# Performance work log

Hardware: AMD Instinct MI355X
Metric: run time of the kernel (lower is better)

## Reference

```python
import jax, jax.numpy as jnp
import numpy as np

N_NODES = 200000
N_GRAPHS = 4000


def _sage_conv(x, src, dst, W_l, b_l, W_r, num_nodes):
    # PyG SAGEConv (aggr='mean'): out = lin_l(mean_{j in N(i)} x_j) + lin_r(x_i)
    msg_sum = jax.ops.segment_sum(x[src], dst, num_segments=num_nodes)      # [N, d]
    deg = jax.ops.segment_sum(jnp.ones_like(src, dtype=x.dtype), dst,
                              num_segments=num_nodes)                       # [N]
    mean_nbr = msg_sum / jnp.maximum(deg, 1.0)[:, None]
    return mean_nbr @ W_l.T + b_l + x @ W_r.T


def setup_inputs() -> dict:
    key = jax.random.key(0)
    ks = jax.random.split(key, 10)
    in_ch, hid, out = 32, 64, 2
    E = 3200000
    x = jax.random.normal(ks[0], (N_NODES, in_ch), dtype=jnp.float32)
    edge_index = jax.random.randint(ks[1], (2, E), 0, N_NODES, dtype=jnp.int64)
    batch = jnp.sort(jax.random.randint(ks[2], (N_NODES,), 0, N_GRAPHS, dtype=jnp.int64))

    def glorot(k, shape):
        lim = 1.0 / np.sqrt(shape[1])
        return jax.random.uniform(k, shape, jnp.float32, -lim, lim)

    return {
        "x": x,
        "edge_index": edge_index,
        "batch": batch,
        "W1_l": glorot(ks[3], (hid, in_ch)),
        "b1": jnp.zeros((hid,), jnp.float32),
        "W1_r": glorot(ks[4], (hid, in_ch)),
        "W2_l": glorot(ks[5], (hid, hid)),
        "b2": jnp.zeros((hid,), jnp.float32),
        "W2_r": glorot(ks[6], (hid, hid)),
        "W_lin": glorot(ks[7], (out, hid)),
        "b_lin": jnp.zeros((out,), jnp.float32),
    }


def reference(x, edge_index, batch, W1_l, b1, W1_r, W2_l, b2, W2_r, W_lin, b_lin):
    src, dst = edge_index[0], edge_index[1]
    h = jax.nn.relu(_sage_conv(x, src, dst, W1_l, b1, W1_r, N_NODES))
    h = jax.nn.relu(_sage_conv(h, src, dst, W2_l, b2, W2_r, N_NODES))
    # global_mean_pool over graph ids
    pool_sum = jax.ops.segment_sum(h, batch, num_segments=N_GRAPHS)          # [G, 64]
    cnt = jax.ops.segment_sum(jnp.ones_like(batch, dtype=h.dtype), batch,
                              num_segments=N_GRAPHS)                          # [G]
    pooled = pool_sum / jnp.maximum(cnt, 1.0)[:, None]
    return pooled @ W_lin.T + b_lin
```

## Files before the change

### kernel.cpp

```cpp
#include <hip/hip_runtime.h>
#include <hip/hip_bf16.h>


#define WS_ALIGN 64
#define EPB 4096
#define BSHIFT 8
#define BNODES 256
#define BCAP 6144
#define MAXNB 1024

typedef short bf16x8 __attribute__((ext_vector_type(8)));
typedef float f32x4 __attribute__((ext_vector_type(4)));

__device__ inline unsigned short f2bf(float f) {
    unsigned u = __float_as_uint(f);
    return (unsigned short)((u + 0x7fffu + ((u >> 16) & 1u)) >> 16);
}

__device__ inline void acc8(const uint4 u, float* a) {
    a[0] += __uint_as_float(u.x << 16);
    a[1] += __uint_as_float(u.x & 0xffff0000u);
    a[2] += __uint_as_float(u.y << 16);
    a[3] += __uint_as_float(u.y & 0xffff0000u);
    a[4] += __uint_as_float(u.z << 16);
    a[5] += __uint_as_float(u.z & 0xffff0000u);
    a[6] += __uint_as_float(u.w << 16);
    a[7] += __uint_as_float(u.w & 0xffff0000u);
}


__global__ void prep_kernel(const float* __restrict__ x, unsigned short* __restrict__ xb,
                            const float* __restrict__ W1_l, const float* __restrict__ W1_r,
                            const float* __restrict__ W2_l, const float* __restrict__ W2_r,
                            unsigned short* __restrict__ whi1, unsigned short* __restrict__ whi2,
                            int* __restrict__ bucketCursor, float* __restrict__ pool,
                            int N, int NB, int G, int total4) {
    const int gid = blockIdx.x * blockDim.x + threadIdx.x;
    if (gid < total4) {
        const float4 v = reinterpret_cast<const float4*>(x)[gid];
        ushort4 o;
        o.x = f2bf(v.x); o.y = f2bf(v.y); o.z = f2bf(v.z); o.w = f2bf(v.w);
        reinterpret_cast<ushort4*>(xb)[gid] = o;
    }
    if (gid < NB) bucketCursor[gid] = gid * BCAP;
    if (gid < G * 64) pool[gid] = 0.0f;
    if (gid < 64 * 64) {
        const int o = gid >> 6, k = gid & 63;
        const float v = (k < 32) ? W1_l[o * 32 + k] : W1_r[o * 32 + (k - 32)];
        whi1[gid] = f2bf(v);
    }
    if (gid < 64 * 128) {
        const int o = gid >> 7, k = gid & 127;
        const float v = (k < 64) ? W2_l[o * 64 + k] : W2_r[o * 64 + (k - 64)];
        whi2[gid] = f2bf(v);
    }
}


__global__ __launch_bounds__(256) void bucket_scatter_kernel(const int* __restrict__ src,
                                                             const int* __restrict__ dst,
                                                             int* __restrict__ bucketCursor,
                                                             unsigned* __restrict__ bucketData,
                                                             int E, int NB) {
    __shared__ int hist[MAXNB];
    __shared__ int cur[MAXNB];
    const int t = threadIdx.x;
    for (int i = t; i < MAXNB; i += 256) hist[i] = 0;
    __syncthreads();
    const int eBase = blockIdx.x * EPB + t;
    int s[16], b[16], dl[16];
#pragma unroll
    for (int j = 0; j < 16; ++j) {
        int e = eBase + j * 256;
        if (e < E) {
            int d = dst[e];
            s[j]  = src[e];
            b[j]  = d >> BSHIFT;
            dl[j] = d & (BNODES - 1);
            atomicAdd(&hist[b[j]], 1);
        } else {
            b[j] = -1;
        }
    }
    __syncthreads();
    for (int bb = t; bb < NB; bb += 256)
        if (hist[bb] > 0) cur[bb] = atomicAdd(&bucketCursor[bb], hist[bb]);
    __syncthreads();
#pragma unroll
    for (int j = 0; j < 16; ++j) {
        if (b[j] >= 0) {
            int pos = atomicAdd(&cur[b[j]], 1);
            if (pos < (b[j] + 1) * BCAP)
                bucketData[pos] = ((unsigned)s[j] << BSHIFT) | (unsigned)dl[j];
        }
    }
}

__global__ __launch_bounds__(256) void csr_build_kernel(const unsigned* __restrict__ bucketData,
                                                        const int* __restrict__ bucketCursor,
                                                        int* __restrict__ offs,
                                                        int* __restrict__ offe,
                                                        int* __restrict__ csr_src,
                                                        int N) {
    __shared__ int cnt[BNODES];
    __shared__ int sscan[BNODES];
    __shared__ int cur[BNODES];
    const int t   = threadIdx.x;
    const int bkt = blockIdx.x;
    const int nodeBase = bkt << BSHIFT;
    const int regionBase = bkt * BCAP;
    const int count = min(bucketCursor[bkt] - regionBase, BCAP);
    cnt[t] = 0;
    __syncthreads();
    for (int k = regionBase + t; k < regionBase + count; k += 256)
        atomicAdd(&cnt[bucketData[k] & (BNODES - 1)], 1);
    __syncthreads();
    int v0 = cnt[t];
    sscan[t] = v0;
    __syncthreads();
    for (int off = 1; off < 256; off <<= 1) {
        int v = (t >= off) ? sscan[t - off] : 0;
        __syncthreads();
        sscan[t] += v;
        __syncthreads();
    }
    const int excl = sscan[t] - v0;
    cur[t] = excl;
    const int node = nodeBase + t;
    if (node < N) {
        offs[node] = regionBase + excl;
        offe[node] = regionBase + excl + v0;
    }
    __syncthreads();
    for (int k = regionBase + t; k < regionBase + count; k += 256) {
        const unsigned v = bucketData[k];
        const int d = (int)(v & (BNODES - 1));
        const int pos = regionBase + atomicAdd(&cur[d], 1);
        csr_src[pos] = (int)(v >> BSHIFT);
    }
}


template <int DIN, bool POOL>
__launch_bounds__(256)
__global__ void fused_agg_mfma_kernel(const unsigned short* __restrict__ featb,
                                      const unsigned short* __restrict__ whi,
                                      const float* __restrict__ bias,
                                      const int* __restrict__ csr_src,
                                      const int* __restrict__ offs,
                                      const int* __restrict__ offe,
                                      unsigned short* __restrict__ houtb,
                                      const int* __restrict__ batch,
                                      float* __restrict__ pool_sum,
                                      int N, int nSteps) {
    constexpr int K     = 2 * DIN;
    constexpr int STR   = K + 8;
    constexpr int D8    = DIN / 8;
    constexpr int NPW   = 64 / D8;
    constexpr int NPASS = 16 / NPW;
    __shared__ unsigned short A_s[64 * STR];
    __shared__ float poolLds[POOL ? 16 * 65 : 1];
    const int tid  = threadIdx.x;
    const int lane = tid & 63;
    const int wave = tid >> 6;
    const int nodeBase = blockIdx.x * 64;
    const int rowBase  = wave * 16;

    if (POOL) {
        for (int i = tid; i < 16 * 65; i += 256) poolLds[i] = 0.0f;
        __syncthreads();
    }

    for (int i = lane; i < 16 * D8; i += 64) {
        const int row = rowBase + i / D8, q = i % D8;
        const int n = min(nodeBase + row, N - 1);
        const uint4 u = *reinterpret_cast<const uint4*>(featb + (size_t)n * DIN + q * 8);
        *reinterpret_cast<uint4*>(&A_s[row * STR + DIN + q * 8]) = u;
    }

    {
        const int part = lane % D8;
        const uint4* base = reinterpret_cast<const uint4*>(featb);
#pragma unroll
        for (int pass = 0; pass < NPASS; ++pass) {
            const int row = rowBase + pass * NPW + lane / D8;
            const int n = nodeBase + row;
            unsigned short* dp = &A_s[row * STR + part * 8];
            if (n < N) {
                const int beg = offs[n];
                const int end = offe[n];
                float a[8] = {0.f, 0.f, 0.f, 0.f, 0.f, 0.f, 0.f, 0.f};
                int k = beg;
                for (; k + 8 <= end; k += 8) {
                    int s[8];
#pragma unroll
                    for (int j = 0; j < 8; ++j) s[j] = csr_src[k + j];
                    uint4 u[8];
#pragma unroll
                    for (int j = 0; j < 8; ++j) u[j] = base[(size_t)s[j] * D8 + part];
#pragma unroll
                    for (int j = 0; j < 8; ++j) acc8(u[j], a);
                }
                for (; k + 4 <= end; k += 4) {
                    const int s0 = csr_src[k + 0];
                    const int s1 = csr_src[k + 1];
                    const int s2 = csr_src[k + 2];
                    const int s3 = csr_src[k + 3];
                    const uint4 u0 = base[(size_t)s0 * D8 + part];
                    const uint4 u1 = base[(size_t)s1 * D8 + part];
                    const uint4 u2 = base[(size_t)s2 * D8 + part];
                    const uint4 u3 = base[(size_t)s3 * D8 + part];
                    acc8(u0, a); acc8(u1, a); acc8(u2, a); acc8(u3, a);
                }
                for (; k < end; ++k) {
                    const uint4 u = base[(size_t)csr_src[k] * D8 + part];
                    acc8(u, a);
                }
                const float inv = 1.0f / fmaxf((float)(end - beg), 1.0f);
                ushort4 lo4, hi4;
                lo4.x = f2bf(a[0] * inv); lo4.y = f2bf(a[1] * inv);
                lo4.z = f2bf(a[2] * inv); lo4.w = f2bf(a[3] * inv);
                hi4.x = f2bf(a[4] * inv); hi4.y = f2bf(a[5] * inv);
                hi4.z = f2bf(a[6] * inv); hi4.w = f2bf(a[7] * inv);
                *reinterpret_cast<ushort4*>(dp)     = lo4;
                *reinterpret_cast<ushort4*>(dp + 4) = hi4;
            } else {
                const ushort4 z = {0, 0, 0, 0};
                *reinterpret_cast<ushort4*>(dp)     = z;
                *reinterpret_cast<ushort4*>(dp + 4) = z;
            }
        }
    }

    asm volatile("s_waitcnt lgkmcnt(0)" ::: "memory");
    __builtin_amdgcn_sched_barrier(0);

    const int lr = lane & 15;
    const int q  = lane >> 4;
    f32x4 acc[4];
#pragma unroll
    for (int t = 0; t < 4; ++t) {
        const float b = bias[t * 16 + lr];
        acc[t] = (f32x4){b, b, b, b};
    }
    const unsigned short* Arow = &A_s[(rowBase + lr) * STR + q * 8];
    const unsigned short* Brow = whi + (size_t)lr * K + q * 8;
    for (int s = 0; s < nSteps; ++s) {
        const bf16x8 af = *reinterpret_cast<const bf16x8*>(Arow + s * 32);
#pragma unroll
        for (int t = 0; t < 4; ++t) {
            const bf16x8 bh = *reinterpret_cast<const bf16x8*>(
                Brow + (size_t)t * 16 * K + s * 32);
            acc[t] = __builtin_amdgcn_mfma_f32_16x16x32_bf16(af, bh, acc[t], 0, 0, 0);
        }
    }

    if (POOL) {
        const int g0 = batch[nodeBase];
        float ag[4] = {0.f, 0.f, 0.f, 0.f};
        int gcur = -1;
        auto flush_run = [&](int g) {
            const int r = g - g0;
            if (r < 16) {
#pragma unroll
                for (int t = 0; t < 4; ++t)
                    atomicAdd(&poolLds[r * 65 + t * 16 + lr], ag[t]);
            } else {
#pragma unroll
                for (int t = 0; t < 4; ++t)
                    atomicAdd(&pool_sum[(size_t)g * 64 + t * 16 + lr], ag[t]);
            }
        };
        for (int reg = 0; reg < 4; ++reg) {
            const int n = nodeBase + rowBase + q * 4 + reg;
            if (n >= N) break;
            const int g = batch[n];
            if (g != gcur) {
                if (gcur >= 0) flush_run(gcur);
                gcur = g;
                ag[0] = ag[1] = ag[2] = ag[3] = 0.f;
            }
#pragma unroll
            for (int t = 0; t < 4; ++t)
                ag[t] += fmaxf(acc[t][reg], 0.0f);
        }
        if (gcur >= 0) flush_run(gcur);
        __syncthreads();
        const int glast = batch[min(nodeBase + 63, N - 1)];
        const int S = min(glast - g0 + 1, 16);
        for (int i = tid; i < S * 64; i += 256) {
            const int r = i >> 6, c = i & 63;
            const float v = poolLds[r * 65 + c];
            float* dstp = &pool_sum[(size_t)(g0 + r) * 64 + c];
            if (r == 0 || r == S - 1) atomicAdd(dstp, v);
            else *dstp = v;
        }
    } else {
        for (int reg = 0; reg < 4; ++reg) {
            const int n = nodeBase + rowBase + q * 4 + reg;
            if (n >= N) break;
#pragma unroll
            for (int t = 0; t < 4; ++t)
                houtb[(size_t)n * 64 + t * 16 + lr] = f2bf(fmaxf(acc[t][reg], 0.0f));
        }
    }
}


__device__ inline int lower_bound_batch(const int* __restrict__ batch, int N, int key) {
    int lo = 0, hi = N;
    while (lo < hi) {
        const int mid = (lo + hi) >> 1;
        if (batch[mid] < key) lo = mid + 1; else hi = mid;
    }
    return lo;
}

__global__ void final_kernel(const float* __restrict__ pool_sum,
                             const int* __restrict__ batch,
                             const float* __restrict__ W_lin,
                             const float* __restrict__ b_lin,
                             float* __restrict__ out, int G, int N) {
    int t = blockIdx.x * blockDim.x + threadIdx.x;
    if (t >= G * 2) return;
    int g = t >> 1, o = t & 1;
    const int c0 = lower_bound_batch(batch, N, g);
    const int c1 = lower_bound_batch(batch, N, g + 1);
    float inv = 1.0f / fmaxf((float)(c1 - c0), 1.0f);
    float acc = b_lin[o];
#pragma unroll
    for (int c = 0; c < 64; ++c)
        acc = fmaf(pool_sum[(size_t)g * 64 + c] * inv, W_lin[o * 64 + c], acc);
    out[t] = acc;
}

extern "C" void kernel_launch(void* const* d_in, const int* in_sizes, int n_in,
                              void* d_out, int out_size, void* d_ws, size_t ws_size,
                              hipStream_t stream) {
    const float* x     = (const float*)d_in[0];
    const int*   ei    = (const int*)d_in[1];
    const int*   batch = (const int*)d_in[2];
    const float* W1_l  = (const float*)d_in[3];
    const float* b1    = (const float*)d_in[4];
    const float* W1_r  = (const float*)d_in[5];
    const float* W2_l  = (const float*)d_in[6];
    const float* b2    = (const float*)d_in[7];
    const float* W2_r  = (const float*)d_in[8];
    const float* W_lin = (const float*)d_in[9];
    const float* b_lin = (const float*)d_in[10];

    const int N = in_sizes[0] / 32;
    const int E = in_sizes[1] / 2;
    const int G = out_size / 2;
    const int* src = ei;
    const int* dst = ei + E;
    const int NB = (N + BNODES - 1) >> BSHIFT;

    char* p = (char*)d_ws;
    auto carve = [&](size_t bytes) -> void* {
        void* r = (void*)p;
        p += (bytes + (WS_ALIGN - 1)) / WS_ALIGN * WS_ALIGN;
        return r;
    };
    int*            bucketCursor = (int*)carve((size_t)MAXNB * 4);
    unsigned*       bucketData   = (unsigned*)carve((size_t)NB * BCAP * 4);
    int*            offs         = (int*)carve((size_t)N * 4);
    int*            offe         = (int*)carve((size_t)N * 4);
    int*            csr_src      = (int*)carve((size_t)NB * BCAP * 4);
    unsigned short* xb           = (unsigned short*)carve((size_t)N * 32 * 2);
    unsigned short* h1b          = (unsigned short*)carve((size_t)N * 64 * 2);
    unsigned short* whi1         = (unsigned short*)carve(64 * 64 * 2);
    unsigned short* whi2         = (unsigned short*)carve(64 * 128 * 2);
    float*          pool         = (float*)carve((size_t)G * 64 * 4);
    float*          out          = (float*)d_out;

    const int TB = 256;
    const int total4 = N * 32 / 4;
    prep_kernel<<<(total4 + TB - 1) / TB, TB, 0, stream>>>(
        x, xb, W1_l, W1_r, W2_l, W2_r, whi1, whi2, bucketCursor, pool,
        N, NB, G, total4);
    bucket_scatter_kernel<<<(E + EPB - 1) / EPB, TB, 0, stream>>>(src, dst, bucketCursor,
                                                                  bucketData, E, NB);
    csr_build_kernel<<<NB, TB, 0, stream>>>(bucketData, bucketCursor, offs, offe, csr_src, N);

    fused_agg_mfma_kernel<32, false><<<(N + 63) / 64, TB, 0, stream>>>(
        xb, whi1, b1, csr_src, offs, offe, h1b, nullptr, nullptr, N, 2);

    fused_agg_mfma_kernel<64, true><<<(N + 63) / 64, TB, 0, stream>>>(
        h1b, whi2, b2, csr_src, offs, offe, nullptr, batch, pool, N, 4);

    final_kernel<<<(G * 2 + TB - 1) / TB, TB, 0, stream>>>(pool, batch, W_lin, b_lin,
                                                           out, G, N);
}
```

Before: 337.0 us.

## Stage bucket scatter and CSR build in LDS for coalesced global writes

The bucket scatter kernel now sorts each block's edge records locally by bucket in shared memory, using a prefix scan over the histogram. It then writes them to global memory in bucket-contiguous order, replacing the earlier random per-edge stores. The CSR build kernel caches the bucket region in LDS, so global memory is read once instead of twice, and it permutes in LDS before writing csr_src out coalesced. This adds significant LDS use: about 48KB in each kernel, which may reduce occupancy. It also adds extra syncthreads and scan passes.

```diff
diff --git a/kernel.cpp b/kernel.cpp
--- a/kernel.cpp
+++ b/kernel.cpp
@@ -63,36 +63,68 @@
                                                              unsigned* __restrict__ bucketData,
                                                              int E, int NB) {
     __shared__ int hist[MAXNB];
-    __shared__ int cur[MAXNB];
+    __shared__ int lofs[MAXNB];
+    __shared__ int lcur[MAXNB];
+    __shared__ int gbase[MAXNB];
+    __shared__ int sscan[256];
+    __shared__ unsigned staged[EPB];
+    __shared__ int gaddr[EPB];
     const int t = threadIdx.x;
     for (int i = t; i < MAXNB; i += 256) hist[i] = 0;
     __syncthreads();
     const int eBase = blockIdx.x * EPB + t;
-    int s[16], b[16], dl[16];
+    int bkt[16]; unsigned rec[16];
 #pragma unroll
     for (int j = 0; j < 16; ++j) {
-        int e = eBase + j * 256;
+        const int e = eBase + j * 256;
         if (e < E) {
-            int d = dst[e];
-            s[j]  = src[e];
-            b[j]  = d >> BSHIFT;
-            dl[j] = d & (BNODES - 1);
-            atomicAdd(&hist[b[j]], 1);
+            const int d = dst[e];
+            bkt[j] = d >> BSHIFT;
+            rec[j] = ((unsigned)src[e] << BSHIFT) | (unsigned)(d & (BNODES - 1));
+            atomicAdd(&hist[bkt[j]], 1);
         } else {
-            b[j] = -1;
-        }
-    }
-    __syncthreads();
+            bkt[j] = -1;
+        }
+    }
+    __syncthreads();
+    const int b4 = t * 4;
+    const int h0 = hist[b4], h1 = hist[b4 + 1], h2 = hist[b4 + 2], h3 = hist[b4 + 3];
+    const int tsum = h0 + h1 + h2 + h3;
+    sscan[t] = tsum;
+    __syncthreads();
+    for (int off = 1; off < 256; off <<= 1) {
+        const int v = (t >= off) ? sscan[t - off] : 0;
+        __syncthreads();
+        sscan[t] += v;
+        __syncthreads();
+    }
+    const int excl = sscan[t] - tsum;
+    lofs[b4]     = excl;
+    lofs[b4 + 1] = excl + h0;
+    lofs[b4 + 2] = excl + h0 + h1;
+    lofs[b4 + 3] = excl + h0 + h1 + h2;
+    lcur[b4]     = lofs[b4];
+    lcur[b4 + 1] = lofs[b4 + 1];
+    lcur[b4 + 2] = lofs[b4 + 2];
+    lcur[b4 + 3] = lofs[b4 + 3];
     for (int bb = t; bb < NB; bb += 256)
-        if (hist[bb] > 0) cur[bb] = atomicAdd(&bucketCursor[bb], hist[bb]);
+        if (hist[bb] > 0) gbase[bb] = atomicAdd(&bucketCursor[bb], hist[bb]);
     __syncthreads();
 #pragma unroll
     for (int j = 0; j < 16; ++j) {
-        if (b[j] >= 0) {
-            int pos = atomicAdd(&cur[b[j]], 1);
-            if (pos < (b[j] + 1) * BCAP)
-                bucketData[pos] = ((unsigned)s[j] << BSHIFT) | (unsigned)dl[j];
-        }
+        if (bkt[j] >= 0) {
+            const int b = bkt[j];
+            const int lp = atomicAdd(&lcur[b], 1);
+            staged[lp] = rec[j];
+            const int gp = gbase[b] + (lp - lofs[b]);
+            gaddr[lp] = (gp < (b + 1) * BCAP) ? gp : -1;
+        }
+    }
+    __syncthreads();
+    const int cnt = min(EPB, E - blockIdx.x * EPB);
+    for (int i = t; i < cnt; i += 256) {
+        const int p = gaddr[i];
+        if (p >= 0) bucketData[p] = staged[i];
     }
 }
 
@@ -102,6 +134,8 @@
                                                         int* __restrict__ offe,
                                                         int* __restrict__ csr_src,
                                                         int N) {
+    __shared__ unsigned ldsIn[BCAP];
+    __shared__ unsigned ldsOut[BCAP];
     __shared__ int cnt[BNODES];
     __shared__ int sscan[BNODES];
     __shared__ int cur[BNODES];
@@ -112,14 +146,17 @@
     const int count = min(bucketCursor[bkt] - regionBase, BCAP);
     cnt[t] = 0;
     __syncthreads();
-    for (int k = regionBase + t; k < regionBase + count; k += 256)
-        atomicAdd(&cnt[bucketData[k] & (BNODES - 1)], 1);
-    __syncthreads();
-    int v0 = cnt[t];
+    for (int k = t; k < count; k += 256) {
+        const unsigned v = bucketData[regionBase + k];
+        ldsIn[k] = v;
+        atomicAdd(&cnt[v & (BNODES - 1)], 1);
+    }
+    __syncthreads();
+    const int v0 = cnt[t];
     sscan[t] = v0;
     __syncthreads();
     for (int off = 1; off < 256; off <<= 1) {
-        int v = (t >= off) ? sscan[t - off] : 0;
+        const int v = (t >= off) ? sscan[t - off] : 0;
         __syncthreads();
         sscan[t] += v;
         __syncthreads();
@@ -132,12 +169,14 @@
         offe[node] = regionBase + excl + v0;
     }
     __syncthreads();
-    for (int k = regionBase + t; k < regionBase + count; k += 256) {
-        const unsigned v = bucketData[k];
-        const int d = (int)(v & (BNODES - 1));
-        const int pos = regionBase + atomicAdd(&cur[d], 1);
-        csr_src[pos] = (int)(v >> BSHIFT);
-    }
+    for (int k = t; k < count; k += 256) {
+        const unsigned v = ldsIn[k];
+        const int p = atomicAdd(&cur[v & (BNODES - 1)], 1);
+        ldsOut[p] = v >> BSHIFT;
+    }
+    __syncthreads();
+    for (int k = t; k < count; k += 256)
+        csr_src[regionBase + k] = (int)ldsOut[k];
 }
 
 
```

Result: faster. 324.7 us (-3.7%).
